# Performance work log

Measured on AMD Instinct MI355X. Metric: run time of the kernel, lower is better.

## Reference

```python
import jax, jax.numpy as jnp
import numpy as np

B, S, H, N = 512, 50, 512, 20000


def setup_inputs() -> dict:
    key = jax.random.key(0)
    ks = jax.random.split(key, 8)
    sc = 1.0 / np.sqrt(H)
    return {
        "all_memory": jax.random.normal(ks[0], (B, S, H), jnp.float32),
        "last_memory": jax.random.normal(ks[1], (B, H), jnp.float32),
        "item_seq": jax.random.randint(ks[2], (B, S), 0, N),
        "mask": jnp.zeros((B, S), dtype=bool),
        "U_w": jax.random.normal(ks[3], (H, H), jnp.float32) * sc,
        "W_w": jax.random.normal(ks[4], (H, H), jnp.float32) * sc,
        "V_w": jax.random.normal(ks[5], (H,), jnp.float32) * sc,
        "V_b": jnp.zeros((1,), jnp.float32),
        "E_w": jax.random.normal(ks[6], (N, 2 * H), jnp.float32) * sc,
    }


def reference(all_memory, last_memory, item_seq, mask, U_w, W_w, V_w, V_b, E_w):
    # Additive (Bahdanau) attention over the basket-sequence memory.
    # torch nn.Linear computes x @ W.T (dropout is identity at eval).
    am = jnp.einsum('bsh,kh->bsk', all_memory, U_w)          # U_explore(all_memory)
    lm = last_memory @ W_w.T                                  # W_explore(last_memory)
    scores = jnp.tanh(am + lm[:, None, :]) @ V_w + V_b[0]     # [B, S]
    scores = jnp.where(mask, -1e9, scores)                    # masked_fill_
    alpha = jax.nn.softmax(scores, axis=1)                    # softmax over seq dim
    ctx = jnp.einsum('bs,bsh->bh', alpha, all_memory)         # attention readout
    feat = jnp.concatenate([ctx, last_memory], axis=-1)       # [B, 2H]
    logits = feat @ E_w.T                                     # [B, N] big GEMM
    # explore_mask = bmm((item_seq>0), one_hot(item_seq)) == scatter-add of counts
    counts = jnp.zeros((B, N), jnp.float32).at[
        jnp.arange(B)[:, None], item_seq
    ].add((item_seq > 0).astype(jnp.float32))
    logits = jnp.where(counts > 0, -jnp.inf, logits)          # mask seen items
    return jax.nn.sigmoid(logits)                             # sigmoid(-inf) -> 0
```

## Files before the change

### kernel.cpp

```cpp
#include <hip/hip_runtime.h>
#include <hip/hip_bf16.h>

#define Bdim 512
#define Sdim 50
#define Hdim 512
#define Ndim 20000
#define Kdim2 1024
#define SEENW 640

typedef __bf16 bf16x8 __attribute__((ext_vector_type(8)));
typedef float f32x4 __attribute__((ext_vector_type(4)));
typedef unsigned short u16;

#define AS1 __attribute__((address_space(1)))
#define AS3 __attribute__((address_space(3)))

__device__ __forceinline__ u16 f2bf(float f) {
  unsigned u = __builtin_bit_cast(unsigned, f);
  u = (u + 0x7fffu + ((u >> 16) & 1u)) >> 16;
  return (u16)u;
}
__device__ __forceinline__ float bf2f(u16 v) {
  unsigned u = ((unsigned)v) << 16;
  return __builtin_bit_cast(float, u);
}
__device__ __forceinline__ unsigned cvt_pk_bf16(float lo, float hi) {
  unsigned r;
  asm("v_cvt_pk_bf16_f32 %0, %1, %2" : "=v"(r) : "v"(lo), "v"(hi));
  return r;
}
__device__ __forceinline__ bf16x8 pack8(float4 lo, float4 hi) {
  union { unsigned u[4]; bf16x8 v; } r;
  r.u[0] = cvt_pk_bf16(lo.x, lo.y);
  r.u[1] = cvt_pk_bf16(lo.z, lo.w);
  r.u[2] = cvt_pk_bf16(hi.x, hi.y);
  r.u[3] = cvt_pk_bf16(hi.z, hi.w);
  return r.v;
}

__global__ __launch_bounds__(256) void prep_kernel(const float* __restrict__ a, u16* __restrict__ da,
                                                   const float* __restrict__ b, u16* __restrict__ db,
                                                   const float* __restrict__ c, u16* __restrict__ dc,
                                                   float* __restrict__ scores, float* __restrict__ lm,
                                                   unsigned* __restrict__ seen) {
  int i = blockIdx.x * blockDim.x + threadIdx.x;
  float4 v; ushort4 o;
  v = reinterpret_cast<const float4*>(a)[i];
  o.x = f2bf(v.x); o.y = f2bf(v.y); o.z = f2bf(v.z); o.w = f2bf(v.w);
  reinterpret_cast<ushort4*>(da)[i] = o;
  v = reinterpret_cast<const float4*>(b)[i];
  o.x = f2bf(v.x); o.y = f2bf(v.y); o.z = f2bf(v.z); o.w = f2bf(v.w);
  reinterpret_cast<ushort4*>(db)[i] = o;
  v = reinterpret_cast<const float4*>(c)[i];
  o.x = f2bf(v.x); o.y = f2bf(v.y); o.z = f2bf(v.z); o.w = f2bf(v.w);
  reinterpret_cast<ushort4*>(dc)[i] = o;
  int stride = gridDim.x * blockDim.x;
  for (int j = i; j < Bdim * Sdim; j += stride) scores[j] = 0.f;
  for (int j = i; j < Bdim * Hdim; j += stride) lm[j] = 0.f;
  for (int j = i; j < Bdim * SEENW; j += stride) seen[j] = 0u;
}

__global__ __launch_bounds__(256) void scatter_kernel(const int* __restrict__ iseq,
                                                      unsigned* __restrict__ seen) {
  int i = blockIdx.x * blockDim.x + threadIdx.x;
  if (i < Bdim * Sdim) {
    int b = i / Sdim;
    int it = iseq[i];
    if (it > 0) atomicOr(&seen[b * SEENW + (it >> 5)], 1u << (it & 31));
  }
}

__global__ __launch_bounds__(256) void softmax_ctx_kernel(
    const float* __restrict__ scores, const unsigned char* __restrict__ mask,
    const float* __restrict__ amF, const float* __restrict__ last_memory,
    u16* __restrict__ feat) {
  int b = blockIdx.x;
  __shared__ float alpha[Sdim];
  int tid = threadIdx.x;
  if (tid < 64) {
    float s = -1e30f;
    if (tid < Sdim) {
      s = scores[b * Sdim + tid];
      if (mask[b * Sdim + tid]) s = -1e9f;
    }
    float m = s;
#pragma unroll
    for (int off = 32; off; off >>= 1) m = fmaxf(m, __shfl_xor(m, off));
    float e = (tid < Sdim) ? __expf(s - m) : 0.f;
    float sum = e;
#pragma unroll
    for (int off = 32; off; off >>= 1) sum += __shfl_xor(sum, off);
    if (tid < Sdim) alpha[tid] = e / sum;
  }
  __syncthreads();
  for (int h = tid; h < Hdim; h += 256) {
    const float* amp = amF + ((long)b * Sdim) * Hdim + h;
    float c = 0.f;
#pragma unroll 5
    for (int s = 0; s < Sdim; ++s) c += alpha[s] * amp[(long)s * Hdim];
    feat[b * Kdim2 + h] = f2bf(c);
    feat[b * Kdim2 + Hdim + h] = f2bf(last_memory[b * Hdim + h]);
  }
}

#define BM 256
#define BN 128
#define BK 32

template <int EPI>
__global__ __launch_bounds__(512, 4) void gemm_bt(
    const u16* __restrict__ A, const u16* __restrict__ Bmat,
    const float* __restrict__ Af,
    int M, int N, int K,
    float* __restrict__ out,
    const float* __restrict__ lm, const float* __restrict__ Vw,
    float* __restrict__ scores) {
  __shared__ bf16x8 Asl[2][BM * BK / 8];
  __shared__ bf16x8 Bsl[2][BN * BK / 8];
  const int tid = threadIdx.x;
  const int lane = tid & 63;
  const int wid = tid >> 6;
  const int wr = wid >> 1, wc = wid & 1;
  const int la = lane & 15, lb = lane >> 4;

  int bx, by, kt0, kt1;
  if constexpr (EPI == 0) {
    bx = blockIdx.x; by = blockIdx.y;
    int ktotal = K / BK; int kper = ktotal / gridDim.z;
    kt0 = blockIdx.z * kper; kt1 = kt0 + kper;
  } else {
    int nwg = gridDim.x, bid = blockIdx.x;
    int q = nwg >> 3, r = nwg & 7;
    int x = bid & 7, i = bid >> 3;
    int wgid = (x < r ? x * (q + 1) : r * (q + 1) + (x - r) * q) + i;
    by = wgid >> 2; bx = wgid & 3;
    kt0 = 0; kt1 = K / BK;
  }
  const int m0 = by * BM;
  const int n0 = bx * BN;

  f32x4 acc[4][4];
  const f32x4 zero = {0.f, 0.f, 0.f, 0.f};
#pragma unroll
  for (int i = 0; i < 4; ++i)
#pragma unroll
    for (int j = 0; j < 4; ++j) acc[i][j] = zero;

  const int rw = tid >> 2;
  const int eA = (tid & 3) * 8;
  const int ch = tid & 3;
  int brB = n0 + rw; if (brB > N - 1) brB = N - 1;

  const u16 *gA0 = nullptr, *gA1 = nullptr, *gB = nullptr;
  const float *gAf0 = nullptr, *gAf1 = nullptr;
  if constexpr (EPI == 1) {
    gAf0 = Af + (long)(m0 + rw) * K + eA;
    gAf1 = Af + (long)(m0 + 128 + rw) * K + eA;
  } else {
    gA0 = A + (long)(m0 + rw) * K + eA;
    gA1 = A + (long)(m0 + 128 + rw) * K + eA;
  }
  gB = Bmat + (long)brB * K + eA;

  float4 ra0, ra1, ra2, ra3;

  auto STAGE_G = [&](int buf, int kt) {
    const int k0 = kt * BK;
    if constexpr (EPI != 1) {
      __builtin_amdgcn_global_load_lds((const AS1 void*)(gA0 + k0),
                                       (AS3 void*)(void*)&Asl[buf][wid * 64], 16, 0, 0);
      __builtin_amdgcn_global_load_lds((const AS1 void*)(gA1 + k0),
                                       (AS3 void*)(void*)&Asl[buf][512 + wid * 64], 16, 0, 0);
    }
    __builtin_amdgcn_global_load_lds((const AS1 void*)(gB + k0),
                                     (AS3 void*)(void*)&Bsl[buf][wid * 64], 16, 0, 0);
  };
  auto LOADR = [&](int kt) {
    const int k0 = kt * BK;
    if constexpr (EPI == 1) {
      ra0 = *reinterpret_cast<const float4*>(gAf0 + k0);
      ra1 = *reinterpret_cast<const float4*>(gAf0 + k0 + 4);
      ra2 = *reinterpret_cast<const float4*>(gAf1 + k0);
      ra3 = *reinterpret_cast<const float4*>(gAf1 + k0 + 4);
    }
  };
  auto WRITER = [&](int buf) {
    if constexpr (EPI == 1) {
      Asl[buf][rw * 4 + ch] = pack8(ra0, ra1);
      Asl[buf][(128 + rw) * 4 + ch] = pack8(ra2, ra3);
    }
  };

  STAGE_G(0, kt0);
  LOADR(kt0);
  WRITER(0);
  __syncthreads();
  int cur = 0;
  for (int kt = kt0; kt < kt1; ++kt) {
    const bool pf = (kt + 1 < kt1);
    if (pf) { STAGE_G(cur ^ 1, kt + 1); LOADR(kt + 1); }

    bf16x8 af[4], bfr[4];
#pragma unroll
    for (int mi = 0; mi < 4; ++mi)
      af[mi] = Asl[cur][(wr * 64 + mi * 16 + la) * 4 + lb];
#pragma unroll
    for (int ni = 0; ni < 4; ++ni)
      bfr[ni] = Bsl[cur][(wc * 64 + ni * 16 + la) * 4 + lb];
#pragma unroll
    for (int mi = 0; mi < 4; ++mi)
#pragma unroll
      for (int ni = 0; ni < 4; ++ni)
        acc[mi][ni] = __builtin_amdgcn_mfma_f32_16x16x32_bf16(af[mi], bfr[ni], acc[mi][ni], 0, 0, 0);

    if (pf) WRITER(cur ^ 1);
    __syncthreads();
    cur ^= 1;
  }

  if constexpr (EPI == 0) {
#pragma unroll
    for (int mi = 0; mi < 4; ++mi)
#pragma unroll
      for (int i = 0; i < 4; ++i) {
        int r = m0 + wr * 64 + mi * 16 + lb * 4 + i;
#pragma unroll
        for (int ni = 0; ni < 4; ++ni) {
          int c = n0 + wc * 64 + ni * 16 + la;
          atomicAdd(&out[(long)r * N + c], acc[mi][ni][i]);
        }
      }
  }
  if constexpr (EPI == 1) {
#pragma unroll
    for (int mi = 0; mi < 4; ++mi)
#pragma unroll
      for (int i = 0; i < 4; ++i) {
        int r = m0 + wr * 64 + mi * 16 + lb * 4 + i;
        int bidx = r / Sdim;
        float p = 0.f;
#pragma unroll
        for (int ni = 0; ni < 4; ++ni) {
          int c = n0 + wc * 64 + ni * 16 + la;
          float x = acc[mi][ni][i] + lm[bidx * Hdim + c];
          x = fminf(fmaxf(x, -9.f), 9.f);
          float e = __expf(2.f * x);
          p += Vw[c] * ((e - 1.f) / (e + 1.f));
        }
        p += __shfl_xor(p, 1);
        p += __shfl_xor(p, 2);
        p += __shfl_xor(p, 4);
        p += __shfl_xor(p, 8);
        if (la == 0) atomicAdd(&scores[r], p);
      }
  }
}

#define LBM 256
#define LBN 128
#define LBK 32

__global__ __launch_bounds__(512, 2) void gemm_logits(
    const u16* __restrict__ A, const float* __restrict__ Bf,
    float* __restrict__ out, const unsigned* __restrict__ seen) {
  __shared__ bf16x8 Asl[3][LBM * LBK / 8];
  __shared__ bf16x8 Bsl[2][LBN * LBK / 8];
  const int tid = threadIdx.x;
  const int lane = tid & 63;
  const int wid = tid >> 6;
  const int wr = wid >> 1, wc = wid & 1;
  const int la = lane & 15, lb = lane >> 4;
  const int kch = lb ^ (la & 3);
  const int K = Kdim2;
  const int NT = K / LBK;

  int nwg = gridDim.x, bid = blockIdx.x;
  int q = nwg >> 3, r = nwg & 7;
  int x = bid & 7, i0 = bid >> 3;
  int wgid = (x < r ? x * (q + 1) : r * (q + 1) + (x - r) * q) + i0;
  const int bx = wgid >> 1, by = wgid & 1;
  const int m0 = by * LBM, n0 = bx * LBN;

  f32x4 acc[4][4];
  const f32x4 zero = {0.f, 0.f, 0.f, 0.f};
#pragma unroll
  for (int i = 0; i < 4; ++i)
#pragma unroll
    for (int j = 0; j < 4; ++j) acc[i][j] = zero;

  const int rw = tid >> 2;
  const int ch = tid & 3;
  const int swz = ch ^ (rw & 3);
  const int chs = swz;
  int brB = n0 + rw; if (brB > Ndim - 1) brB = Ndim - 1;
  const u16* gA0 = A + (long)(m0 + rw) * K + swz * 8;
  const u16* gA1 = A + (long)(m0 + 128 + rw) * K + swz * 8;
  const float* gBf = Bf + (long)brB * K + ch * 8;

  auto STAGE_A = [&](int kt, int slot) {
    const int k0 = kt * LBK;
    __builtin_amdgcn_global_load_lds((const AS1 void*)(gA0 + k0),
                                     (AS3 void*)(void*)&Asl[slot][wid * 64], 16, 0, 0);
    __builtin_amdgcn_global_load_lds((const AS1 void*)(gA1 + k0),
                                     (AS3 void*)(void*)&Asl[slot][512 + wid * 64], 16, 0, 0);
  };
  auto COMP = [&](int slA, int slB) {
    bf16x8 af[4], bfr[4];
#pragma unroll
    for (int mi = 0; mi < 4; ++mi)
      af[mi] = Asl[slA][(wr * 64 + mi * 16 + la) * 4 + kch];
#pragma unroll
    for (int ni = 0; ni < 4; ++ni)
      bfr[ni] = Bsl[slB][(wc * 64 + ni * 16 + la) * 4 + kch];
#pragma unroll
    for (int mi = 0; mi < 4; ++mi)
#pragma unroll
      for (int ni = 0; ni < 4; ++ni)
        acc[mi][ni] = __builtin_amdgcn_mfma_f32_16x16x32_bf16(af[mi], bfr[ni], acc[mi][ni], 0, 0, 0);
  };

  float4 b0lo, b0hi, b1lo, b1hi;

  STAGE_A(0, 0);
  __builtin_amdgcn_sched_barrier(0);
  b0lo = *reinterpret_cast<const float4*>(gBf);
  b0hi = *reinterpret_cast<const float4*>(gBf + 4);
  __builtin_amdgcn_sched_barrier(0);
  STAGE_A(1, 1);
  __builtin_amdgcn_sched_barrier(0);
  b1lo = *reinterpret_cast<const float4*>(gBf + LBK);
  b1hi = *reinterpret_cast<const float4*>(gBf + LBK + 4);
  Bsl[0][rw * 4 + chs] = pack8(b0lo, b0hi);
  asm volatile("s_waitcnt vmcnt(4) lgkmcnt(0)" ::: "memory");
  __builtin_amdgcn_sched_barrier(0);
  __builtin_amdgcn_s_barrier();
  __builtin_amdgcn_sched_barrier(0);

  auto ITER = [&](int kt, float4& ldlo, float4& ldhi, float4& stlo, float4& sthi) {
    int tpf = kt + 2; if (tpf > NT - 1) tpf = NT - 1;
    STAGE_A(tpf, (kt + 2) % 3);
    __builtin_amdgcn_sched_barrier(0);
    ldlo = *reinterpret_cast<const float4*>(gBf + tpf * LBK);
    ldhi = *reinterpret_cast<const float4*>(gBf + tpf * LBK + 4);
    COMP(kt % 3, kt & 1);
    Bsl[(kt + 1) & 1][rw * 4 + chs] = pack8(stlo, sthi);
    asm volatile("s_waitcnt vmcnt(4) lgkmcnt(0)" ::: "memory");
    __builtin_amdgcn_sched_barrier(0);
    __builtin_amdgcn_s_barrier();
    __builtin_amdgcn_sched_barrier(0);
  };

  for (int kt = 0; kt < NT; kt += 2) {
    ITER(kt,     b0lo, b0hi, b1lo, b1hi);
    ITER(kt + 1, b1lo, b1hi, b0lo, b0hi);
  }

#pragma unroll
  for (int mi = 0; mi < 4; ++mi)
#pragma unroll
    for (int i = 0; i < 4; ++i) {
      int r = m0 + wr * 64 + mi * 16 + lb * 4 + i;
      long rb = (long)r * Ndim;
#pragma unroll
      for (int ni = 0; ni < 4; ++ni) {
        int c = n0 + wc * 64 + ni * 16 + la;
        if (c < Ndim) {
          unsigned wbits = seen[r * SEENW + (c >> 5)];
          float val = 0.f;
          if (!((wbits >> (c & 31)) & 1u))
            val = 1.f / (1.f + __expf(-acc[mi][ni][i]));
          out[rb + c] = val;
        }
      }
    }
}

extern "C" void kernel_launch(void* const* d_in, const int* in_sizes, int n_in,
                              void* d_out, int out_size, void* d_ws, size_t ws_size,
                              hipStream_t stream) {
  (void)in_sizes; (void)n_in; (void)out_size; (void)ws_size;
  const float* all_memory  = (const float*)d_in[0];
  const float* last_memory = (const float*)d_in[1];
  const int*   item_seq    = (const int*)d_in[2];
  const unsigned char* mask = (const unsigned char*)d_in[3];
  const float* U_w = (const float*)d_in[4];
  const float* W_w = (const float*)d_in[5];
  const float* V_w = (const float*)d_in[6];
  const float* E_w = (const float*)d_in[8];
  float* out = (float*)d_out;

  char* w = (char*)d_ws;
  u16* wsFeat = (u16*)w; w += (size_t)Bdim * Kdim2 * 2;
  u16* wsLast = (u16*)w; w += (size_t)Hdim * Hdim * 2;
  u16* wsW    = (u16*)w; w += (size_t)Hdim * Hdim * 2;
  u16* wsU    = (u16*)w; w += (size_t)Hdim * Hdim * 2;
  float* wsLm     = (float*)w; w += (size_t)Bdim * Hdim * 4;
  float* wsScores = (float*)w; w += (size_t)Bdim * Sdim * 4;
  unsigned* wsSeen = (unsigned*)w; w += (size_t)Bdim * SEENW * 4;

  prep_kernel<<<256, 256, 0, stream>>>(last_memory, wsLast, W_w, wsW, U_w, wsU,
                                       wsScores, wsLm, wsSeen);
  scatter_kernel<<<100, 256, 0, stream>>>(item_seq, wsSeen);

  gemm_bt<0><<<dim3(Hdim / BN, Bdim / BM, 4), 512, 0, stream>>>(
      wsLast, wsW, nullptr, Bdim, Hdim, Hdim, wsLm, nullptr, nullptr, nullptr);
  gemm_bt<1><<<dim3((Bdim * Sdim / BM) * (Hdim / BN)), 512, 0, stream>>>(
      nullptr, wsU, all_memory, Bdim * Sdim, Hdim, Hdim, nullptr,
      wsLm, V_w, wsScores);
  softmax_ctx_kernel<<<Bdim, 256, 0, stream>>>(wsScores, mask, all_memory, last_memory, wsFeat);
  gemm_logits<<<dim3(((Ndim + LBN - 1) / LBN) * (Bdim / LBM)), 512, 0, stream>>>(
      wsFeat, E_w, out, wsSeen);
}
```

Before: 120.9 us.

## Load GEMM fragments directly from global memory, dropping LDS staging pipeline

Replaces the LDS-staged, triple/double-buffered logits GEMM with a loop in which each wave loads its A (bf16) and B (fp32, packed to bf16) MFMA fragments straight from global memory. All shared-memory buffers, barriers and explicit waitcnt scheduling are removed, and the launch-bounds occupancy hint is relaxed. The aim is to cut barrier and LDS overhead. The cost is redundant global/L2 traffic, since the two waves that share rows or columns each fetch the same data, and the loop loses its explicit prefetch overlap.

```diff
diff --git a/kernel.cpp b/kernel.cpp
--- a/kernel.cpp
+++ b/kernel.cpp
@@ -258,21 +258,15 @@
 
 #define LBM 256
 #define LBN 128
-#define LBK 32
-
-__global__ __launch_bounds__(512, 2) void gemm_logits(
+
+__global__ __launch_bounds__(512) void gemm_logits(
     const u16* __restrict__ A, const float* __restrict__ Bf,
     float* __restrict__ out, const unsigned* __restrict__ seen) {
-  __shared__ bf16x8 Asl[3][LBM * LBK / 8];
-  __shared__ bf16x8 Bsl[2][LBN * LBK / 8];
   const int tid = threadIdx.x;
   const int lane = tid & 63;
   const int wid = tid >> 6;
   const int wr = wid >> 1, wc = wid & 1;
   const int la = lane & 15, lb = lane >> 4;
-  const int kch = lb ^ (la & 3);
-  const int K = Kdim2;
-  const int NT = K / LBK;
 
   int nwg = gridDim.x, bid = blockIdx.x;
   int q = nwg >> 3, r = nwg & 7;
@@ -288,71 +282,36 @@
 #pragma unroll
     for (int j = 0; j < 4; ++j) acc[i][j] = zero;
 
-  const int rw = tid >> 2;
-  const int ch = tid & 3;
-  const int swz = ch ^ (rw & 3);
-  const int chs = swz;
-  int brB = n0 + rw; if (brB > Ndim - 1) brB = Ndim - 1;
-  const u16* gA0 = A + (long)(m0 + rw) * K + swz * 8;
-  const u16* gA1 = A + (long)(m0 + 128 + rw) * K + swz * 8;
-  const float* gBf = Bf + (long)brB * K + ch * 8;
-
-  auto STAGE_A = [&](int kt, int slot) {
-    const int k0 = kt * LBK;
-    __builtin_amdgcn_global_load_lds((const AS1 void*)(gA0 + k0),
-                                     (AS3 void*)(void*)&Asl[slot][wid * 64], 16, 0, 0);
-    __builtin_amdgcn_global_load_lds((const AS1 void*)(gA1 + k0),
-                                     (AS3 void*)(void*)&Asl[slot][512 + wid * 64], 16, 0, 0);
-  };
-  auto COMP = [&](int slA, int slB) {
+  const u16* pa[4];
+  const float* pb[4];
+#pragma unroll
+  for (int mi = 0; mi < 4; ++mi)
+    pa[mi] = A + (long)(m0 + wr * 64 + mi * 16 + la) * Kdim2 + lb * 8;
+#pragma unroll
+  for (int ni = 0; ni < 4; ++ni) {
+    int rr = n0 + wc * 64 + ni * 16 + la;
+    if (rr > Ndim - 1) rr = Ndim - 1;
+    pb[ni] = Bf + (long)rr * Kdim2 + lb * 8;
+  }
+
+#pragma unroll 2
+  for (int kt = 0; kt < Kdim2 / 32; ++kt) {
+    const int k0 = kt * 32;
     bf16x8 af[4], bfr[4];
 #pragma unroll
-    for (int mi = 0; mi < 4; ++mi)
-      af[mi] = Asl[slA][(wr * 64 + mi * 16 + la) * 4 + kch];
-#pragma unroll
-    for (int ni = 0; ni < 4; ++ni)
-      bfr[ni] = Bsl[slB][(wc * 64 + ni * 16 + la) * 4 + kch];
+    for (int ni = 0; ni < 4; ++ni) {
+      float4 lo = *reinterpret_cast<const float4*>(pb[ni] + k0);
+      float4 hi = *reinterpret_cast<const float4*>(pb[ni] + k0 + 4);
+      bfr[ni] = pack8(lo, hi);
+    }
+#pragma unroll
+    for (int mi = 0; mi < 4; ++mi)
+      af[mi] = *reinterpret_cast<const bf16x8*>(pa[mi] + k0);
 #pragma unroll
     for (int mi = 0; mi < 4; ++mi)
 #pragma unroll
       for (int ni = 0; ni < 4; ++ni)
         acc[mi][ni] = __builtin_amdgcn_mfma_f32_16x16x32_bf16(af[mi], bfr[ni], acc[mi][ni], 0, 0, 0);
-  };
-
-  float4 b0lo, b0hi, b1lo, b1hi;
-
-  STAGE_A(0, 0);
-  __builtin_amdgcn_sched_barrier(0);
-  b0lo = *reinterpret_cast<const float4*>(gBf);
-  b0hi = *reinterpret_cast<const float4*>(gBf + 4);
-  __builtin_amdgcn_sched_barrier(0);
-  STAGE_A(1, 1);
-  __builtin_amdgcn_sched_barrier(0);
-  b1lo = *reinterpret_cast<const float4*>(gBf + LBK);
-  b1hi = *reinterpret_cast<const float4*>(gBf + LBK + 4);
-  Bsl[0][rw * 4 + chs] = pack8(b0lo, b0hi);
-  asm volatile("s_waitcnt vmcnt(4) lgkmcnt(0)" ::: "memory");
-  __builtin_amdgcn_sched_barrier(0);
-  __builtin_amdgcn_s_barrier();
-  __builtin_amdgcn_sched_barrier(0);
-
-  auto ITER = [&](int kt, float4& ldlo, float4& ldhi, float4& stlo, float4& sthi) {
-    int tpf = kt + 2; if (tpf > NT - 1) tpf = NT - 1;
-    STAGE_A(tpf, (kt + 2) % 3);
-    __builtin_amdgcn_sched_barrier(0);
-    ldlo = *reinterpret_cast<const float4*>(gBf + tpf * LBK);
-    ldhi = *reinterpret_cast<const float4*>(gBf + tpf * LBK + 4);
-    COMP(kt % 3, kt & 1);
-    Bsl[(kt + 1) & 1][rw * 4 + chs] = pack8(stlo, sthi);
-    asm volatile("s_waitcnt vmcnt(4) lgkmcnt(0)" ::: "memory");
-    __builtin_amdgcn_sched_barrier(0);
-    __builtin_amdgcn_s_barrier();
-    __builtin_amdgcn_sched_barrier(0);
-  };
-
-  for (int kt = 0; kt < NT; kt += 2) {
-    ITER(kt,     b0lo, b0hi, b1lo, b1hi);
-    ITER(kt + 1, b1lo, b1hi, b0lo, b0hi);
   }
 
 #pragma unroll
```

After: 254.5 us. 2.1x slower.

## Deepen B-operand register prefetch to four buffers in logits GEMM

Applied to the files above, without the earlier changes.

The fp32 E_w operand is now prefetched into registers three k-tiles ahead, using four register buffers instead of two, and the main loop is unrolled by four. Shared-memory slot indices rotate through counters instead of modulo arithmetic, the vmcnt waits are retuned to match the new number of loads in flight, and a final vmcnt(0) drains outstanding loads. The aim is to hide global-load latency on the B stream behind more MFMA work. The extra live float4 registers add pressure under launch_bounds(512,2), which could cause spills or lower occupancy.

```diff
diff --git a/kernel.cpp b/kernel.cpp
--- a/kernel.cpp
+++ b/kernel.cpp
@@ -271,8 +271,7 @@
   const int wr = wid >> 1, wc = wid & 1;
   const int la = lane & 15, lb = lane >> 4;
   const int kch = lb ^ (la & 3);
-  const int K = Kdim2;
-  const int NT = K / LBK;
+  const int NT = Kdim2 / LBK;
 
   int nwg = gridDim.x, bid = blockIdx.x;
   int q = nwg >> 3, r = nwg & 7;
@@ -291,19 +290,24 @@
   const int rw = tid >> 2;
   const int ch = tid & 3;
   const int swz = ch ^ (rw & 3);
-  const int chs = swz;
   int brB = n0 + rw; if (brB > Ndim - 1) brB = Ndim - 1;
-  const u16* gA0 = A + (long)(m0 + rw) * K + swz * 8;
-  const u16* gA1 = A + (long)(m0 + 128 + rw) * K + swz * 8;
-  const float* gBf = Bf + (long)brB * K + ch * 8;
+  const u16* gA0 = A + (long)(m0 + rw) * Kdim2 + swz * 8;
+  const u16* gA1 = A + (long)(m0 + 128 + rw) * Kdim2 + swz * 8;
+  const float* gBf = Bf + (long)brB * Kdim2 + ch * 8;
 
   auto STAGE_A = [&](int kt, int slot) {
-    const int k0 = kt * LBK;
+    int t = kt > NT - 1 ? NT - 1 : kt;
+    const int k0 = t * LBK;
     __builtin_amdgcn_global_load_lds((const AS1 void*)(gA0 + k0),
                                      (AS3 void*)(void*)&Asl[slot][wid * 64], 16, 0, 0);
     __builtin_amdgcn_global_load_lds((const AS1 void*)(gA1 + k0),
                                      (AS3 void*)(void*)&Asl[slot][512 + wid * 64], 16, 0, 0);
   };
+  auto BLOAD = [&](int kt, float4& lo, float4& hi) {
+    int t = kt > NT - 1 ? NT - 1 : kt;
+    lo = *reinterpret_cast<const float4*>(gBf + t * LBK);
+    hi = *reinterpret_cast<const float4*>(gBf + t * LBK + 4);
+  };
   auto COMP = [&](int slA, int slB) {
     bf16x8 af[4], bfr[4];
 #pragma unroll
@@ -319,41 +323,46 @@
         acc[mi][ni] = __builtin_amdgcn_mfma_f32_16x16x32_bf16(af[mi], bfr[ni], acc[mi][ni], 0, 0, 0);
   };
 
-  float4 b0lo, b0hi, b1lo, b1hi;
+  float4 b0lo, b0hi, b1lo, b1hi, b2lo, b2hi, b3lo, b3hi;
 
   STAGE_A(0, 0);
-  __builtin_amdgcn_sched_barrier(0);
-  b0lo = *reinterpret_cast<const float4*>(gBf);
-  b0hi = *reinterpret_cast<const float4*>(gBf + 4);
-  __builtin_amdgcn_sched_barrier(0);
   STAGE_A(1, 1);
   __builtin_amdgcn_sched_barrier(0);
-  b1lo = *reinterpret_cast<const float4*>(gBf + LBK);
-  b1hi = *reinterpret_cast<const float4*>(gBf + LBK + 4);
-  Bsl[0][rw * 4 + chs] = pack8(b0lo, b0hi);
-  asm volatile("s_waitcnt vmcnt(4) lgkmcnt(0)" ::: "memory");
+  BLOAD(0, b0lo, b0hi);
+  BLOAD(1, b1lo, b1hi);
+  BLOAD(2, b2lo, b2hi);
+  BLOAD(3, b3lo, b3hi);
+  __builtin_amdgcn_sched_barrier(0);
+  Bsl[0][rw * 4 + swz] = pack8(b0lo, b0hi);
+  asm volatile("s_waitcnt vmcnt(10) lgkmcnt(0)" ::: "memory");
   __builtin_amdgcn_sched_barrier(0);
   __builtin_amdgcn_s_barrier();
   __builtin_amdgcn_sched_barrier(0);
 
+  int sC = 0, sS = 2;
   auto ITER = [&](int kt, float4& ldlo, float4& ldhi, float4& stlo, float4& sthi) {
-    int tpf = kt + 2; if (tpf > NT - 1) tpf = NT - 1;
-    STAGE_A(tpf, (kt + 2) % 3);
+    STAGE_A(kt + 2, sS);
     __builtin_amdgcn_sched_barrier(0);
-    ldlo = *reinterpret_cast<const float4*>(gBf + tpf * LBK);
-    ldhi = *reinterpret_cast<const float4*>(gBf + tpf * LBK + 4);
-    COMP(kt % 3, kt & 1);
-    Bsl[(kt + 1) & 1][rw * 4 + chs] = pack8(stlo, sthi);
-    asm volatile("s_waitcnt vmcnt(4) lgkmcnt(0)" ::: "memory");
+    BLOAD(kt + 4, ldlo, ldhi);
+    __builtin_amdgcn_sched_barrier(0);
+    COMP(sC, kt & 1);
+    __builtin_amdgcn_sched_barrier(0);
+    Bsl[(kt + 1) & 1][rw * 4 + swz] = pack8(stlo, sthi);
+    asm volatile("s_waitcnt vmcnt(6) lgkmcnt(0)" ::: "memory");
     __builtin_amdgcn_sched_barrier(0);
     __builtin_amdgcn_s_barrier();
     __builtin_amdgcn_sched_barrier(0);
-  };
-
-  for (int kt = 0; kt < NT; kt += 2) {
+    sC = (sC == 2) ? 0 : sC + 1;
+    sS = (sS == 2) ? 0 : sS + 1;
+  };
+
+  for (int kt = 0; kt < NT; kt += 4) {
     ITER(kt,     b0lo, b0hi, b1lo, b1hi);
-    ITER(kt + 1, b1lo, b1hi, b0lo, b0hi);
-  }
+    ITER(kt + 1, b1lo, b1hi, b2lo, b2hi);
+    ITER(kt + 2, b2lo, b2hi, b3lo, b3hi);
+    ITER(kt + 3, b3lo, b3hi, b0lo, b0hi);
+  }
+  asm volatile("s_waitcnt vmcnt(0)" ::: "memory");
 
 #pragma unroll
   for (int mi = 0; mi < 4; ++mi)
```

Result: slower. 165.0 us (+36.4%).
